# Kernel optimization log

Hardware: AMD Instinct MI355X
Metric: run time of the kernel (lower is better)

The kernel has to match this reference:

```python
import jax, jax.numpy as jnp
import numpy as np

NUM_RELATIONS = 8
N_NODES = 50000
N_EDGES = 640000
D_IN = 128
D_HID = 128
N_CLASSES = 16


def rgcn_layer(x, edge_index, edge_type, edge_weight, W):
    # Faithful to ExtendedRGCNConv.forward: per-relation propagate with
    # message = (edge_weight * x_j) @ W[rel]  (== edge_weight * (x_j @ W[rel]))
    # aggregated by scatter-MEAN (PyG RGCNConv default aggr), summed over relations.
    # No root weight / bias (the override skips them).
    src, dst = edge_index[0], edge_index[1]
    num_nodes = x.shape[0]
    out = jnp.zeros((num_nodes, W.shape[2]), dtype=x.dtype)
    for r in range(W.shape[0]):
        sel = edge_type == r
        w = jnp.where(sel, edge_weight, jnp.zeros((), x.dtype))  # [E]
        h = x @ W[r]                                             # [N, out]
        msg = h[src] * w[:, None]                                # [E, out]
        s = jax.ops.segment_sum(msg, dst, num_segments=num_nodes)
        cnt = jax.ops.segment_sum(sel.astype(x.dtype), dst, num_segments=num_nodes)
        out = out + s / jnp.maximum(cnt, 1.0)[:, None]
    return out


def setup_inputs() -> dict:
    key = jax.random.key(0)
    k1, k2, k3, k4, k5, k6 = jax.random.split(key, 6)
    x = jax.random.normal(k1, (N_NODES, D_IN), dtype=jnp.float32)
    edge_index = jax.random.randint(k2, (2, N_EDGES), 0, N_NODES, dtype=jnp.int64)
    edge_type = jax.random.randint(k3, (N_EDGES,), 0, NUM_RELATIONS, dtype=jnp.int64)
    edge_attr = jax.random.uniform(k4, (N_EDGES,), dtype=jnp.float32)
    # Xavier-uniform-ish relation weight banks
    b1 = (6.0 / (D_IN + D_HID)) ** 0.5
    W1 = jax.random.uniform(k5, (NUM_RELATIONS, D_IN, D_HID), minval=-b1, maxval=b1, dtype=jnp.float32)
    b2 = (6.0 / (D_HID + N_CLASSES)) ** 0.5
    W2 = jax.random.uniform(k6, (NUM_RELATIONS, D_HID, N_CLASSES), minval=-b2, maxval=b2, dtype=jnp.float32)
    return {"x": x, "edge_index": edge_index, "edge_type": edge_type, "edge_attr": edge_attr, "W1": W1, "W2": W2}


def reference(x, edge_index, edge_type, edge_attr, W1, W2):
    h = rgcn_layer(x, edge_index, edge_type, edge_attr, W1)
    h = jax.nn.relu(h)
    h = rgcn_layer(h, edge_index, edge_type, edge_attr, W2)
    return jax.nn.log_softmax(h, axis=1)
```

## Files before the change

### kernel.cpp

```cpp
#include <hip/hip_runtime.h>
#include <hip/hip_bf16.h>
#include <math.h>

#define NN 50000
#define EE 640000
#define DD 128
#define NREL 8
#define NCLS 16
#define NBUCK (NREL * NN)
#define SCAN_NB ((NBUCK + 255) / 256)
#define RECCAP 40

typedef __attribute__((ext_vector_type(8))) short short8;
typedef __attribute__((ext_vector_type(4))) float f32x4;

__device__ __forceinline__ float bflo(unsigned u) { return __uint_as_float(u << 16); }
__device__ __forceinline__ float bfhi(unsigned u) { return __uint_as_float(u & 0xffff0000u); }
__device__ __forceinline__ float bf2f(ushort u) { return __uint_as_float(((unsigned)u) << 16); }
__device__ __forceinline__ ushort f2b(float f) {
  unsigned u = __float_as_uint(f);
  u += 0x7fff + ((u >> 16) & 1);
  return (ushort)(u >> 16);
}

#define XQ (NN * DD / 4)
#define PACKN (XQ + NREL * DD * DD + DD * DD)
__global__ __launch_bounds__(256) void countpack_kernel(const int* __restrict__ ei,
                                                        const int* __restrict__ et,
                                                        const float* __restrict__ x,
                                                        const float* __restrict__ W1,
                                                        const float* __restrict__ W2,
                                                        int* __restrict__ cnt,
                                                        ushort* __restrict__ xb,
                                                        ushort* __restrict__ W1Tc,
                                                        ushort* __restrict__ W2T) {
  int t = blockIdx.x * 256 + threadIdx.x;
  if (t < EE) {
    int key = ei[EE + t] * NREL + et[t];
    atomicAdd(&cnt[key], 1);
  }
  if (t < XQ) {
    float4 v = *(const float4*)&x[(size_t)t * 4];
    *(ushort4*)&xb[(size_t)t * 4] = make_ushort4(f2b(v.x), f2b(v.y), f2b(v.z), f2b(v.w));
  } else if (t < XQ + NREL * DD * DD) {
    int t2 = t - XQ;
    int n = t2 >> 10, r = (t2 >> 7) & 7, k = t2 & 127;
    W1Tc[t2] = f2b(W1[r * 16384 + k * 128 + n]);
  } else if (t < PACKN) {
    int t2 = t - XQ - NREL * DD * DD;
    int j = t2 >> 7, k = t2 & 127;
    W2T[t2] = f2b(W2[(j >> 4) * (DD * NCLS) + k * NCLS + (j & 15)]);
  }
}

__global__ __launch_bounds__(256) void scan1_kernel(const int* __restrict__ cnt,
                                                    int* __restrict__ off,
                                                    int* __restrict__ bsum) {
  __shared__ int s[256];
  const int tid = threadIdx.x;
  const int i = blockIdx.x * 256 + tid;
  int v = (i < NBUCK) ? cnt[i] : 0;
  s[tid] = v;
  __syncthreads();
#pragma unroll
  for (int o = 1; o < 256; o <<= 1) {
    int t2 = (tid >= o) ? s[tid - o] : 0;
    __syncthreads();
    s[tid] += t2;
    __syncthreads();
  }
  if (i < NBUCK) off[i] = s[tid] - v;
  if (tid == 255) bsum[blockIdx.x] = s[255];
}

__global__ __launch_bounds__(64) void scan2_kernel(const int* __restrict__ bsum,
                                                   int* __restrict__ bpre) {
  const int lane = threadIdx.x;
  int carry = 0;
  for (int base = 0; base < SCAN_NB; base += 64) {
    int idx = base + lane;
    int own = (idx < SCAN_NB) ? bsum[idx] : 0;
    int v = own;
#pragma unroll
    for (int o = 1; o < 64; o <<= 1) {
      int t = __shfl_up(v, o, 64);
      if (lane >= o) v += t;
    }
    if (idx < SCAN_NB) bpre[idx] = carry + v - own;
    carry += __shfl(v, 63, 64);
  }
}

__global__ __launch_bounds__(256) void scan3_kernel(int* __restrict__ off,
                                                    const int* __restrict__ bpre,
                                                    int* __restrict__ cursor) {
  int i = blockIdx.x * 256 + threadIdx.x;
  if (i < NBUCK) {
    int o = off[i] + bpre[i >> 8];
    off[i] = o;
    cursor[i] = o;
  }
  if (i == 0) off[NBUCK] = EE;
}

__global__ __launch_bounds__(256) void bucket_kernel(const int* __restrict__ ei,
                                                     const int* __restrict__ et,
                                                     const float* __restrict__ ew,
                                                     const int* __restrict__ cnt,
                                                     int* __restrict__ cursor,
                                                     uint2* __restrict__ rec) {
  int e = blockIdx.x * 256 + threadIdx.x;
  if (e >= EE) return;
  int r = et[e];
  int key = ei[EE + e] * NREL + r;
  float scale = ew[e] / fmaxf((float)cnt[key], 1.0f);
  int pos = atomicAdd(&cursor[key], 1);
  rec[pos] = make_uint2((unsigned)ei[e] | ((unsigned)r << 16), __float_as_uint(scale));
}

__global__ __launch_bounds__(512) void fused1_kernel(const int* __restrict__ off,
                                                     const uint2* __restrict__ rec,
                                                     const ushort* __restrict__ xb,
                                                     const ushort* __restrict__ W1Tc,
                                                     const ushort* __restrict__ W2T,
                                                     ushort* __restrict__ H2) {
  __shared__ ushort AsU[64 * 136];
  __shared__ uint2 recL[64 * RECCAP];
  const int tid = threadIdx.x;
  const int m0 = blockIdx.x * 64;
  const int wave = tid >> 6, lane = tid & 63;
  const int lm = lane & 15, lkb = (lane >> 4) * 8;
  const int gn = tid >> 3;
  const int gj = tid & 7;
  const int gc = gj * 16;
  const int v = m0 + gn;

  int offv[9];
  if (v < NN) {
    int4 o0 = *(const int4*)&off[v * 8];
    int4 o1 = *(const int4*)&off[v * 8 + 4];
    offv[0] = o0.x; offv[1] = o0.y; offv[2] = o0.z; offv[3] = o0.w;
    offv[4] = o1.x; offv[5] = o1.y; offv[6] = o1.z; offv[7] = o1.w;
    offv[8] = off[v * 8 + 8];
  } else {
#pragma unroll
    for (int i = 0; i < 9; i++) offv[i] = 0;
  }
  const int b0 = offv[0];
  const int rbase = gn * RECCAP;
  {
    int dcap = min(offv[8] - b0, RECCAP);
    for (int i = gj; i < dcap; i += 8) recL[rbase + i] = rec[b0 + i];
  }

#define GETREC(qdst, ii)                                        \
  do {                                                          \
    int _ri = (ii) - b0;                                        \
    if (_ri < RECCAP) qdst = recL[rbase + _ri];                 \
    else qdst = rec[(ii)];                                      \
  } while (0)

  f32x4 acc[4];
#pragma unroll
  for (int m = 0; m < 4; m++) acc[m] = (f32x4){0.f, 0.f, 0.f, 0.f};

#pragma unroll
  for (int r = 0; r < NREL; r++) {
    __syncthreads();
    float g[16];
#pragma unroll
    for (int j = 0; j < 16; j++) g[j] = 0.f;
    {
      int s = offv[r], e = offv[r + 1];
      int i = s;
      for (; i + 2 <= e; i += 2) {
        uint2 q0, q1;
        GETREC(q0, i);
        GETREC(q1, i + 1);
        float sc0 = __uint_as_float(q0.y), sc1 = __uint_as_float(q1.y);
        const ushort* xr0 = &xb[(size_t)(q0.x & 0xffff) * DD + gc];
        const ushort* xr1 = &xb[(size_t)(q1.x & 0xffff) * DD + gc];
        uint4 h0[2], h1[2];
#pragma unroll
        for (int jj = 0; jj < 2; jj++) h0[jj] = *(const uint4*)&xr0[jj * 8];
#pragma unroll
        for (int jj = 0; jj < 2; jj++) h1[jj] = *(const uint4*)&xr1[jj * 8];
#pragma unroll
        for (int jj = 0; jj < 2; jj++) {
          float* gg = &g[jj * 8];
          gg[0] = fmaf(sc0, bflo(h0[jj].x), gg[0]);
          gg[1] = fmaf(sc0, bfhi(h0[jj].x), gg[1]);
          gg[2] = fmaf(sc0, bflo(h0[jj].y), gg[2]);
          gg[3] = fmaf(sc0, bfhi(h0[jj].y), gg[3]);
          gg[4] = fmaf(sc0, bflo(h0[jj].z), gg[4]);
          gg[5] = fmaf(sc0, bfhi(h0[jj].z), gg[5]);
          gg[6] = fmaf(sc0, bflo(h0[jj].w), gg[6]);
          gg[7] = fmaf(sc0, bfhi(h0[jj].w), gg[7]);
          gg[0] = fmaf(sc1, bflo(h1[jj].x), gg[0]);
          gg[1] = fmaf(sc1, bfhi(h1[jj].x), gg[1]);
          gg[2] = fmaf(sc1, bflo(h1[jj].y), gg[2]);
          gg[3] = fmaf(sc1, bfhi(h1[jj].y), gg[3]);
          gg[4] = fmaf(sc1, bflo(h1[jj].z), gg[4]);
          gg[5] = fmaf(sc1, bfhi(h1[jj].z), gg[5]);
          gg[6] = fmaf(sc1, bflo(h1[jj].w), gg[6]);
          gg[7] = fmaf(sc1, bfhi(h1[jj].w), gg[7]);
        }
      }
      if (i < e) {
        uint2 q;
        GETREC(q, i);
        float sc = __uint_as_float(q.y);
        const ushort* xr = &xb[(size_t)(q.x & 0xffff) * DD + gc];
#pragma unroll
        for (int jj = 0; jj < 2; jj++) {
          uint4 h = *(const uint4*)&xr[jj * 8];
          float* gg = &g[jj * 8];
          gg[0] = fmaf(sc, bflo(h.x), gg[0]);
          gg[1] = fmaf(sc, bfhi(h.x), gg[1]);
          gg[2] = fmaf(sc, bflo(h.y), gg[2]);
          gg[3] = fmaf(sc, bfhi(h.y), gg[3]);
          gg[4] = fmaf(sc, bflo(h.z), gg[4]);
          gg[5] = fmaf(sc, bfhi(h.z), gg[5]);
          gg[6] = fmaf(sc, bflo(h.w), gg[6]);
          gg[7] = fmaf(sc, bfhi(h.w), gg[7]);
        }
      }
    }
#pragma unroll
    for (int jj = 0; jj < 2; jj++) {
      uint4 u;
      u.x = (unsigned)f2b(g[jj * 8 + 0]) | ((unsigned)f2b(g[jj * 8 + 1]) << 16);
      u.y = (unsigned)f2b(g[jj * 8 + 2]) | ((unsigned)f2b(g[jj * 8 + 3]) << 16);
      u.z = (unsigned)f2b(g[jj * 8 + 4]) | ((unsigned)f2b(g[jj * 8 + 5]) << 16);
      u.w = (unsigned)f2b(g[jj * 8 + 6]) | ((unsigned)f2b(g[jj * 8 + 7]) << 16);
      *(uint4*)&AsU[gn * 136 + gc + jj * 8] = u;
    }
    __syncthreads();
#pragma unroll
    for (int k0 = 0; k0 < 128; k0 += 32) {
      short8 b = *(const short8*)&W1Tc[(size_t)(wave * 16 + lm) * 1024 + r * 128 + k0 + lkb];
      short8 a[4];
#pragma unroll
      for (int m = 0; m < 4; m++)
        a[m] = *(const short8*)&AsU[(m * 16 + lm) * 136 + k0 + lkb];
#pragma unroll
      for (int m = 0; m < 4; m++)
        acc[m] = __builtin_amdgcn_mfma_f32_16x16x32_bf16(a[m], b, acc[m], 0, 0, 0);
    }
  }
#undef GETREC

  __syncthreads();
  const int rquad = (lane >> 4) * 4;
#pragma unroll
  for (int m = 0; m < 4; m++)
#pragma unroll
    for (int i = 0; i < 4; i++)
      AsU[(m * 16 + rquad + i) * 136 + wave * 16 + lm] = f2b(fmaxf(acc[m][i], 0.f));
  __syncthreads();

  f32x4 acc2[4];
#pragma unroll
  for (int m = 0; m < 4; m++) acc2[m] = (f32x4){0.f, 0.f, 0.f, 0.f};
#pragma unroll
  for (int k0 = 0; k0 < 128; k0 += 32) {
    short8 b = *(const short8*)&W2T[(size_t)(wave * 16 + lm) * DD + k0 + lkb];
    short8 a[4];
#pragma unroll
    for (int m = 0; m < 4; m++)
      a[m] = *(const short8*)&AsU[(m * 16 + lm) * 136 + k0 + lkb];
#pragma unroll
    for (int m = 0; m < 4; m++)
      acc2[m] = __builtin_amdgcn_mfma_f32_16x16x32_bf16(a[m], b, acc2[m], 0, 0, 0);
  }
  __syncthreads();
#pragma unroll
  for (int m = 0; m < 4; m++)
#pragma unroll
    for (int i = 0; i < 4; i++)
      AsU[(m * 16 + rquad + i) * 136 + wave * 16 + lm] = f2b(acc2[m][i]);
  __syncthreads();
#pragma unroll
  for (int i = 0; i < 2; i++) {
    int seg = tid + i * 512;
    int row = seg >> 4, c8 = (seg & 15) * 8;
    int gr = m0 + row;
    if (gr < NN) *(uint4*)&H2[(size_t)gr * DD + c8] = *(const uint4*)&AsU[row * 136 + c8];
  }
}

__global__ __launch_bounds__(256) void gather2_kernel(const int* __restrict__ off,
                                                      const uint2* __restrict__ rec,
                                                      const ushort* __restrict__ H2,
                                                      float* __restrict__ out) {
  __shared__ uint2 recL[8 * RECCAP];
  const int tid = threadIdx.x;
  const int g = tid >> 5;
  const int sub = tid & 31;
  const int j = sub >> 4;
  const int c = sub & 15;
  const int v = blockIdx.x * 8 + g;
  int s = 0, e = 0;
  if (v < NN) {
    s = off[v * NREL];
    e = off[v * NREL + NREL];
  }
  const int rbase = g * RECCAP;
  {
    int dcap = min(e - s, RECCAP);
    for (int i = sub; i < dcap; i += 32) recL[rbase + i] = rec[s + i];
  }
  __syncthreads();

#define GETREC2(qdst, ii)                                       \
  do {                                                          \
    int _ri = (ii) - s;                                         \
    if (_ri < RECCAP) qdst = recL[rbase + _ri];                 \
    else qdst = rec[(ii)];                                      \
  } while (0)

  float acc = 0.f;
  if (v < NN) {
    int i = s + j;
    for (; i + 2 < e; i += 4) {
      uint2 q0, q1;
      GETREC2(q0, i);
      GETREC2(q1, i + 2);
      ushort h0 = H2[(size_t)(q0.x & 0xffff) * DD + (q0.x >> 16) * NCLS + c];
      ushort h1 = H2[(size_t)(q1.x & 0xffff) * DD + (q1.x >> 16) * NCLS + c];
      acc = fmaf(__uint_as_float(q0.y), bf2f(h0), acc);
      acc = fmaf(__uint_as_float(q1.y), bf2f(h1), acc);
    }
    for (; i < e; i += 2) {
      uint2 q;
      GETREC2(q, i);
      acc = fmaf(__uint_as_float(q.y),
                 bf2f(H2[(size_t)(q.x & 0xffff) * DD + (q.x >> 16) * NCLS + c]), acc);
    }
  }
#undef GETREC2
  acc += __shfl_xor(acc, 16, 32);
  float m = acc;
#pragma unroll
  for (int mask = 8; mask >= 1; mask >>= 1) m = fmaxf(m, __shfl_xor(m, mask, 16));
  float ex = expf(acc - m);
#pragma unroll
  for (int mask = 8; mask >= 1; mask >>= 1) ex += __shfl_xor(ex, mask, 16);
  if (v < NN && j == 0) out[(size_t)v * NCLS + c] = acc - m - logf(ex);
}

extern "C" void kernel_launch(void* const* d_in, const int* in_sizes, int n_in,
                              void* d_out, int out_size, void* d_ws, size_t ws_size,
                              hipStream_t stream) {
  const float* x  = (const float*)d_in[0];
  const int*   ei = (const int*)d_in[1];
  const int*   et = (const int*)d_in[2];
  const float* ew = (const float*)d_in[3];
  const float* W1 = (const float*)d_in[4];
  const float* W2 = (const float*)d_in[5];
  float* out = (float*)d_out;
  float* ws = (float*)d_ws;

  int*    cnt    = (int*)ws;
  int*    off    = (int*)(ws + 400000);
  int*    bsum   = (int*)(ws + 800004);
  int*    bpre   = (int*)(ws + 801568);
  int*    cursor = (int*)(ws + 803132);
  uint2*  rec    = (uint2*)(ws + 1203132);
  ushort* xb     = (ushort*)(ws + 2483132);
  ushort* W1Tc   = (ushort*)(ws + 5683132);
  ushort* W2T    = (ushort*)(ws + 5748668);
  ushort* H2     = (ushort*)(ws + 5756860);

  hipMemsetAsync(cnt, 0, (size_t)NBUCK * sizeof(int), stream);

  countpack_kernel<<<(PACKN + 255) / 256, 256, 0, stream>>>(ei, et, x, W1, W2, cnt, xb, W1Tc, W2T);
  scan1_kernel<<<SCAN_NB, 256, 0, stream>>>(cnt, off, bsum);
  scan2_kernel<<<1, 64, 0, stream>>>(bsum, bpre);
  scan3_kernel<<<SCAN_NB, 256, 0, stream>>>(off, bpre, cursor);
  bucket_kernel<<<(EE + 255) / 256, 256, 0, stream>>>(ei, et, ew, cnt, cursor, rec);

  fused1_kernel<<<(NN + 63) / 64, 512, 0, stream>>>(off, rec, xb, W1Tc, W2T, H2);
  gather2_kernel<<<(NN + 7) / 8, 256, 0, stream>>>(off, rec, H2, out);
}
```

Before: 257.1 us.

## Replace three-pass global scan with per-node wave scan and atomic base allocation

The three scan kernels are replaced by one kernel. It prefix-sums each node's 8 relation counts in registers, scans node degrees within a wave, and reserves a contiguous range with one atomicAdd per wave, so node segments sit in arbitrary order rather than sorted order. The bucket kernel then reuses the count array with atomicSub as the cursor and derives the degree from the offsets, which removes the separate cursor array and two launches. Offsets are stored with a stride of 12 per node. Because the wave ranges are nondeterministic, the edge layout varies from run to run and locality across neighbouring nodes may drop.

```diff
diff --git a/kernel.cpp b/kernel.cpp
--- a/kernel.cpp
+++ b/kernel.cpp
@@ -8,8 +8,8 @@
 #define NREL 8
 #define NCLS 16
 #define NBUCK (NREL * NN)
-#define SCAN_NB ((NBUCK + 255) / 256)
 #define RECCAP 40
+#define OSTR 12
 
 typedef __attribute__((ext_vector_type(8))) short short8;
 typedef __attribute__((ext_vector_type(4))) float f32x4;
@@ -53,72 +53,65 @@
   }
 }
 
-__global__ __launch_bounds__(256) void scan1_kernel(const int* __restrict__ cnt,
-                                                    int* __restrict__ off,
-                                                    int* __restrict__ bsum) {
-  __shared__ int s[256];
-  const int tid = threadIdx.x;
-  const int i = blockIdx.x * 256 + tid;
-  int v = (i < NBUCK) ? cnt[i] : 0;
-  s[tid] = v;
-  __syncthreads();
-#pragma unroll
-  for (int o = 1; o < 256; o <<= 1) {
-    int t2 = (tid >= o) ? s[tid - o] : 0;
-    __syncthreads();
-    s[tid] += t2;
-    __syncthreads();
-  }
-  if (i < NBUCK) off[i] = s[tid] - v;
-  if (tid == 255) bsum[blockIdx.x] = s[255];
-}
-
-__global__ __launch_bounds__(64) void scan2_kernel(const int* __restrict__ bsum,
-                                                   int* __restrict__ bpre) {
-  const int lane = threadIdx.x;
-  int carry = 0;
-  for (int base = 0; base < SCAN_NB; base += 64) {
-    int idx = base + lane;
-    int own = (idx < SCAN_NB) ? bsum[idx] : 0;
-    int v = own;
-#pragma unroll
-    for (int o = 1; o < 64; o <<= 1) {
-      int t = __shfl_up(v, o, 64);
-      if (lane >= o) v += t;
-    }
-    if (idx < SCAN_NB) bpre[idx] = carry + v - own;
-    carry += __shfl(v, 63, 64);
-  }
-}
-
-__global__ __launch_bounds__(256) void scan3_kernel(int* __restrict__ off,
-                                                    const int* __restrict__ bpre,
-                                                    int* __restrict__ cursor) {
-  int i = blockIdx.x * 256 + threadIdx.x;
-  if (i < NBUCK) {
-    int o = off[i] + bpre[i >> 8];
-    off[i] = o;
-    cursor[i] = o;
-  }
-  if (i == 0) off[NBUCK] = EE;
+__global__ __launch_bounds__(256) void base_kernel(const int* __restrict__ cnt,
+                                                   int* __restrict__ gcur,
+                                                   int* __restrict__ offN) {
+  const int v = blockIdx.x * 256 + threadIdx.x;
+  const int lane = threadIdx.x & 63;
+  int pre[9];
+  pre[0] = 0;
+  int deg = 0;
+  if (v < NN) {
+    int4 c0 = *(const int4*)&cnt[v * 8];
+    int4 c1 = *(const int4*)&cnt[v * 8 + 4];
+    pre[1] = pre[0] + c0.x;
+    pre[2] = pre[1] + c0.y;
+    pre[3] = pre[2] + c0.z;
+    pre[4] = pre[3] + c0.w;
+    pre[5] = pre[4] + c1.x;
+    pre[6] = pre[5] + c1.y;
+    pre[7] = pre[6] + c1.z;
+    pre[8] = pre[7] + c1.w;
+    deg = pre[8];
+  } else {
+#pragma unroll
+    for (int i = 1; i < 9; i++) pre[i] = 0;
+  }
+  int incl = deg;
+#pragma unroll
+  for (int o = 1; o < 64; o <<= 1) {
+    int t = __shfl_up(incl, o, 64);
+    if (lane >= o) incl += t;
+  }
+  int wtotal = __shfl(incl, 63, 64);
+  int wbase = 0;
+  if (lane == 63) wbase = atomicAdd(gcur, wtotal);
+  wbase = __shfl(wbase, 63, 64);
+  if (v < NN) {
+    int nbase = wbase + incl - deg;
+#pragma unroll
+    for (int i = 0; i < 9; i++) offN[v * OSTR + i] = nbase + pre[i];
+  }
 }
 
 __global__ __launch_bounds__(256) void bucket_kernel(const int* __restrict__ ei,
                                                      const int* __restrict__ et,
                                                      const float* __restrict__ ew,
-                                                     const int* __restrict__ cnt,
-                                                     int* __restrict__ cursor,
+                                                     const int* __restrict__ offN,
+                                                     int* __restrict__ cnt,
                                                      uint2* __restrict__ rec) {
   int e = blockIdx.x * 256 + threadIdx.x;
   if (e >= EE) return;
   int r = et[e];
-  int key = ei[EE + e] * NREL + r;
-  float scale = ew[e] / fmaxf((float)cnt[key], 1.0f);
-  int pos = atomicAdd(&cursor[key], 1);
+  int v = ei[EE + e];
+  int b0 = offN[v * OSTR + r];
+  int b1 = offN[v * OSTR + r + 1];
+  float scale = ew[e] / fmaxf((float)(b1 - b0), 1.0f);
+  int pos = b0 + atomicSub(&cnt[v * NREL + r], 1) - 1;
   rec[pos] = make_uint2((unsigned)ei[e] | ((unsigned)r << 16), __float_as_uint(scale));
 }
 
-__global__ __launch_bounds__(512) void fused1_kernel(const int* __restrict__ off,
+__global__ __launch_bounds__(512) void fused1_kernel(const int* __restrict__ offN,
                                                      const uint2* __restrict__ rec,
                                                      const ushort* __restrict__ xb,
                                                      const ushort* __restrict__ W1Tc,
@@ -137,11 +130,11 @@
 
   int offv[9];
   if (v < NN) {
-    int4 o0 = *(const int4*)&off[v * 8];
-    int4 o1 = *(const int4*)&off[v * 8 + 4];
+    int4 o0 = *(const int4*)&offN[v * OSTR];
+    int4 o1 = *(const int4*)&offN[v * OSTR + 4];
     offv[0] = o0.x; offv[1] = o0.y; offv[2] = o0.z; offv[3] = o0.w;
     offv[4] = o1.x; offv[5] = o1.y; offv[6] = o1.z; offv[7] = o1.w;
-    offv[8] = off[v * 8 + 8];
+    offv[8] = offN[v * OSTR + 8];
   } else {
 #pragma unroll
     for (int i = 0; i < 9; i++) offv[i] = 0;
@@ -289,7 +282,7 @@
   }
 }
 
-__global__ __launch_bounds__(256) void gather2_kernel(const int* __restrict__ off,
+__global__ __launch_bounds__(256) void gather2_kernel(const int* __restrict__ offN,
                                                       const uint2* __restrict__ rec,
                                                       const ushort* __restrict__ H2,
                                                       float* __restrict__ out) {
@@ -302,8 +295,8 @@
   const int v = blockIdx.x * 8 + g;
   int s = 0, e = 0;
   if (v < NN) {
-    s = off[v * NREL];
-    e = off[v * NREL + NREL];
+    s = offN[v * OSTR];
+    e = offN[v * OSTR + 8];
   }
   const int rbase = g * RECCAP;
   {
@@ -361,25 +354,21 @@
   float* out = (float*)d_out;
   float* ws = (float*)d_ws;
 
-  int*    cnt    = (int*)ws;
-  int*    off    = (int*)(ws + 400000);
-  int*    bsum   = (int*)(ws + 800004);
-  int*    bpre   = (int*)(ws + 801568);
-  int*    cursor = (int*)(ws + 803132);
-  uint2*  rec    = (uint2*)(ws + 1203132);
-  ushort* xb     = (ushort*)(ws + 2483132);
-  ushort* W1Tc   = (ushort*)(ws + 5683132);
-  ushort* W2T    = (ushort*)(ws + 5748668);
-  ushort* H2     = (ushort*)(ws + 5756860);
-
-  hipMemsetAsync(cnt, 0, (size_t)NBUCK * sizeof(int), stream);
+  int*    cnt  = (int*)ws;
+  int*    gcur = (int*)(ws + 400000);
+  int*    offN = (int*)(ws + 400004);
+  uint2*  rec  = (uint2*)(ws + 1000004);
+  ushort* xb   = (ushort*)(ws + 2280004);
+  ushort* W1Tc = (ushort*)(ws + 5480004);
+  ushort* W2T  = (ushort*)(ws + 5545540);
+  ushort* H2   = (ushort*)(ws + 5553732);
+
+  hipMemsetAsync(cnt, 0, (size_t)(NBUCK + 1) * sizeof(int), stream);
 
   countpack_kernel<<<(PACKN + 255) / 256, 256, 0, stream>>>(ei, et, x, W1, W2, cnt, xb, W1Tc, W2T);
-  scan1_kernel<<<SCAN_NB, 256, 0, stream>>>(cnt, off, bsum);
-  scan2_kernel<<<1, 64, 0, stream>>>(bsum, bpre);
-  scan3_kernel<<<SCAN_NB, 256, 0, stream>>>(off, bpre, cursor);
-  bucket_kernel<<<(EE + 255) / 256, 256, 0, stream>>>(ei, et, ew, cnt, cursor, rec);
-
-  fused1_kernel<<<(NN + 63) / 64, 512, 0, stream>>>(off, rec, xb, W1Tc, W2T, H2);
-  gather2_kernel<<<(NN + 7) / 8, 256, 0, stream>>>(off, rec, H2, out);
-}
+  base_kernel<<<(NN + 255) / 256, 256, 0, stream>>>(cnt, gcur, offN);
+  bucket_kernel<<<(EE + 255) / 256, 256, 0, stream>>>(ei, et, ew, offN, cnt, rec);
+
+  fused1_kernel<<<(NN + 63) / 64, 512, 0, stream>>>(offN, rec, xb, W1Tc, W2T, H2);
+  gather2_kernel<<<(NN + 7) / 8, 256, 0, stream>>>(offN, rec, H2, out);
+}
```

After: 250.1 us. -2.7%, faster.
